# Optimization experiments

Hardware: AMD Instinct MI355X
Metric: run time of the kernel (lower is better)

Reference implementation:

```python
import jax, jax.numpy as jnp
import numpy as np

B, D, H, W, K = 32, 128, 128, 128, 32

def setup_inputs() -> dict:
    key = jax.random.key(0)
    k1, k2, k3 = jax.random.split(key, 3)
    X = jax.random.normal(k1, (B, D, H, W), dtype=jnp.float32)
    std1 = 1.0 / np.sqrt(K * D)
    codewords = jax.random.uniform(k2, (K, D), dtype=jnp.float32, minval=-std1, maxval=std1)
    scale = jax.random.uniform(k3, (K,), dtype=jnp.float32, minval=-1.0, maxval=0.0)
    return {"X": X, "codewords": codewords, "scale": scale}

def reference(X, codewords, scale):
    # X: [B, D, H, W] -> [B, N, D]
    b, d = X.shape[0], X.shape[1]
    x = X.reshape(b, d, -1).transpose(0, 2, 1)  # [B, N, D]
    x2 = jnp.sum(x * x, axis=-1, keepdims=True)            # [B, N, 1]
    c2 = jnp.sum(codewords * codewords, axis=-1)           # [K]
    xc = jnp.einsum('bnd,kd->bnk', x, codewords)           # [B, N, K]
    sl = scale * (x2 - 2.0 * xc + c2)                      # [B, N, K]
    A = jax.nn.softmax(sl, axis=2)                         # assignment weights
    # E[b,k,d] = sum_n A[b,n,k] * (x[b,n,d] - c[k,d])
    E = jnp.einsum('bnk,bnd->bkd', A, x) - jnp.sum(A, axis=1)[..., None] * codewords
    return E
```

## Files before the change

kernel.cpp:

```cpp
#include <hip/hip_runtime.h>
#include <hip/hip_bf16.h>

#define B_   32
#define D_   128
#define N_   16384
#define K_   32
#define NS   128
#define XS_STRIDE 136
#define AST_STRIDE 136

#define WS_WBF  0
#define WS_SC   2048
#define WS_C2S  2080
#define WS_EP   2112

typedef __attribute__((ext_vector_type(8))) short bf16x8;
typedef __attribute__((ext_vector_type(4))) float f32x4;

static __device__ inline unsigned int pk2(float lo, float hi) {
    __hip_bfloat162 h = __float22bfloat162_rn(make_float2(lo, hi));
    unsigned int r;
    __builtin_memcpy(&r, &h, 4);
    return r;
}

static __device__ inline bf16x8 pack8v(f32x4 a, f32x4 b) {
    union { unsigned int u[4]; bf16x8 f; } r;
    r.u[0] = pk2(a[0], a[1]);
    r.u[1] = pk2(a[2], a[3]);
    r.u[2] = pk2(b[0], b[1]);
    r.u[3] = pk2(b[2], b[3]);
    return r.f;
}

__global__ void prep_kernel(const float* __restrict__ cw,
                            const float* __restrict__ scale,
                            float* __restrict__ ws) {
    const int k = blockIdx.x;
    const int l = threadIdx.x;
    const float sc = scale[k] * 1.44269504088896f;
    unsigned short* Wbf = (unsigned short*)(ws + WS_WBF);
    float s = 0.f;
#pragma unroll
    for (int i = 0; i < 2; ++i) {
        const int d = l + i * 64;
        const float v = cw[k * D_ + d];
        s += v * v;
        const float w = -2.f * sc * v;
        unsigned int u = __float_as_uint(w);
        u += 0x7fffu + ((u >> 16) & 1u);
        Wbf[k * D_ + d] = (unsigned short)(u >> 16);
    }
#pragma unroll
    for (int o = 32; o > 0; o >>= 1) s += __shfl_down(s, o, 64);
    if (l == 0) {
        ws[WS_SC  + k] = sc;
        ws[WS_C2S + k] = sc * s;
    }
}

template<int NCHUNKT>
__global__ __launch_bounds__(256, 3) void main_kernel(
        const float* __restrict__ X,
        const float* __restrict__ ws_ro,
        float* __restrict__ AsumP,
        float* __restrict__ Ep)
{
    constexpr int CSZT  = N_ / NCHUNKT;
    constexpr int NSUBT = CSZT / NS;

    __shared__ __align__(16) unsigned short Xs[NS * XS_STRIDE];
    __shared__ __align__(16) unsigned short AsT[K_ * AST_STRIDE];

    const int t    = threadIdx.x;
    const int lane = t & 63;
    const int w    = t >> 6;
    const int mc   = lane & 15;
    const int q    = lane >> 4;

    const int blk   = blockIdx.x;
    const int b     = blk / NCHUNKT;
    const int chunk = blk % NCHUNKT;
    const int n0    = chunk * CSZT;

    const float* Xb = X + (size_t)b * ((size_t)D_ * N_);

    const unsigned short* Wbf = (const unsigned short*)(ws_ro + WS_WBF);
    bf16x8 wf[2][4];
#pragma unroll
    for (int kb = 0; kb < 2; ++kb)
#pragma unroll
        for (int kd = 0; kd < 4; ++kd)
            wf[kb][kd] = *(const bf16x8*)&Wbf[(kb * 16 + mc) * D_ + kd * 32 + q * 8];

    float scr[2][4], c2r[2][4];
#pragma unroll
    for (int kb = 0; kb < 2; ++kb)
#pragma unroll
        for (int r = 0; r < 4; ++r) {
            scr[kb][r] = ws_ro[WS_SC  + kb * 16 + q * 4 + r];
            c2r[kb][r] = ws_ro[WS_C2S + kb * 16 + q * 4 + r];
        }

    bf16x8 ones;
#pragma unroll
    for (int i = 0; i < 8; ++i) ones[i] = (short)0x3F80;

    f32x4 accE[2][2] = {{{0.f,0.f,0.f,0.f},{0.f,0.f,0.f,0.f}},
                        {{0.f,0.f,0.f,0.f},{0.f,0.f,0.f,0.f}}};
    f32x4 accO[2]    = {{0.f,0.f,0.f,0.f},{0.f,0.f,0.f,0.f}};

    const float* xr0 = Xb + (size_t)(w * 32 + mc) * N_ + n0 + q * 8;
    const int dA = w * 32 + mc;

    for (int s = 0; s < NSUBT; ++s) {
        const float* xp = xr0 + s * NS;
        bf16x8 xf0[4], xf1[4];
#pragma unroll
        for (int ks = 0; ks < 4; ++ks) {
            const f32x4 a0 = *(const f32x4*)(xp + ks * 32);
            const f32x4 b0 = *(const f32x4*)(xp + ks * 32 + 4);
            const f32x4 a1 = *(const f32x4*)(xp + ks * 32 + (size_t)16 * N_);
            const f32x4 b1 = *(const f32x4*)(xp + ks * 32 + (size_t)16 * N_ + 4);
            xf0[ks] = pack8v(a0, b0);
            xf1[ks] = pack8v(a1, b1);
        }
#pragma unroll
        for (int ks = 0; ks < 4; ++ks) {
            union { bf16x8 f; unsigned int u[4]; } ua, ub;
            ua.f = xf0[ks];
            ub.f = xf1[ks];
            const int base = (ks * 32 + q * 8) * XS_STRIDE + dA;
#pragma unroll
            for (int j2 = 0; j2 < 4; ++j2) {
                Xs[base + (2*j2)   * XS_STRIDE]      = (unsigned short)(ua.u[j2]);
                Xs[base + (2*j2+1) * XS_STRIDE]      = (unsigned short)(ua.u[j2] >> 16);
                Xs[base + (2*j2)   * XS_STRIDE + 16] = (unsigned short)(ub.u[j2]);
                Xs[base + (2*j2+1) * XS_STRIDE + 16] = (unsigned short)(ub.u[j2] >> 16);
            }
        }
        __syncthreads();

#pragma unroll
        for (int cb = 0; cb < NS / 64; ++cb) {
            const int ntl  = (w * (NS / 64) + cb) * 16;
            const int rowb = (ntl + mc) * XS_STRIDE;

            union fr { bf16x8 f; unsigned int u[4]; } xb[4];
#pragma unroll
            for (int kd = 0; kd < 4; ++kd)
                xb[kd].f = *(const bf16x8*)&Xs[rowb + kd * 32 + q * 8];

            float x2 = 0.f;
#pragma unroll
            for (int kd = 0; kd < 4; ++kd)
#pragma unroll
                for (int wd = 0; wd < 4; ++wd) {
                    const float lo = __uint_as_float(xb[kd].u[wd] << 16);
                    const float hi = __uint_as_float(xb[kd].u[wd] & 0xffff0000u);
                    x2 = fmaf(lo, lo, x2);
                    x2 = fmaf(hi, hi, x2);
                }

            f32x4 S0 = {0.f,0.f,0.f,0.f};
            f32x4 S1 = {0.f,0.f,0.f,0.f};
#pragma unroll
            for (int kd = 0; kd < 4; ++kd) {
                S0 = __builtin_amdgcn_mfma_f32_16x16x32_bf16(wf[0][kd], xb[kd].f, S0, 0, 0, 0);
                S1 = __builtin_amdgcn_mfma_f32_16x16x32_bf16(wf[1][kd], xb[kd].f, S1, 0, 0, 0);
            }

            x2 += __shfl_xor(x2, 16, 64);
            x2 += __shfl_xor(x2, 32, 64);

            float sl[8];
#pragma unroll
            for (int r = 0; r < 4; ++r) {
                sl[r]     = fmaf(scr[0][r], x2, S0[r] + c2r[0][r]);
                sl[4 + r] = fmaf(scr[1][r], x2, S1[r] + c2r[1][r]);
            }
            float m = sl[0];
#pragma unroll
            for (int i = 1; i < 8; ++i) m = fmaxf(m, sl[i]);
            m = fmaxf(m, __shfl_xor(m, 16, 64));
            m = fmaxf(m, __shfl_xor(m, 32, 64));
            float ssum = 0.f;
#pragma unroll
            for (int i = 0; i < 8; ++i) { sl[i] = exp2f(sl[i] - m); ssum += sl[i]; }
            ssum += __shfl_xor(ssum, 16, 64);
            ssum += __shfl_xor(ssum, 32, 64);
            const float inv = 1.f / ssum;

            const int col = ntl + mc;
#pragma unroll
            for (int r = 0; r < 4; ++r) {
                const unsigned int u = pk2(sl[r] * inv, sl[4 + r] * inv);
                AsT[(q * 4 + r) * AST_STRIDE + col]      = (unsigned short)u;
                AsT[(16 + q * 4 + r) * AST_STRIDE + col] = (unsigned short)(u >> 16);
            }
        }
        __syncthreads();

#pragma unroll
        for (int ks = 0; ks < NS / 32; ++ks) {
            const int nl = ks * 32 + q * 8;
            const bf16x8 a0 = *(const bf16x8*)&AsT[mc * AST_STRIDE + nl];
            const bf16x8 a1 = *(const bf16x8*)&AsT[(16 + mc) * AST_STRIDE + nl];
            accE[0][0] = __builtin_amdgcn_mfma_f32_16x16x32_bf16(a0, xf0[ks], accE[0][0], 0, 0, 0);
            accE[0][1] = __builtin_amdgcn_mfma_f32_16x16x32_bf16(a0, xf1[ks], accE[0][1], 0, 0, 0);
            accE[1][0] = __builtin_amdgcn_mfma_f32_16x16x32_bf16(a1, xf0[ks], accE[1][0], 0, 0, 0);
            accE[1][1] = __builtin_amdgcn_mfma_f32_16x16x32_bf16(a1, xf1[ks], accE[1][1], 0, 0, 0);
            if (w == 0) {
                accO[0] = __builtin_amdgcn_mfma_f32_16x16x32_bf16(a0, ones, accO[0], 0, 0, 0);
                accO[1] = __builtin_amdgcn_mfma_f32_16x16x32_bf16(a1, ones, accO[1], 0, 0, 0);
            }
        }
    }

    float* EpB = Ep + (size_t)blk * (K_ * D_);
#pragma unroll
    for (int kh = 0; kh < 2; ++kh)
#pragma unroll
        for (int ds = 0; ds < 2; ++ds)
#pragma unroll
            for (int r = 0; r < 4; ++r) {
                const int k = kh * 16 + q * 4 + r;
                const int d = w * 32 + ds * 16 + mc;
                EpB[k * D_ + d] = accE[kh][ds][r];
            }
    if (w == 0 && mc == 0) {
#pragma unroll
        for (int kh = 0; kh < 2; ++kh)
#pragma unroll
            for (int r = 0; r < 4; ++r)
                AsumP[blk * K_ + kh * 16 + q * 4 + r] = accO[kh][r];
    }
}

template<int NCHUNKT>
__global__ void finalize_kernel(const float* __restrict__ cw,
                                const float* __restrict__ AsumP,
                                const float* __restrict__ Ep,
                                float* __restrict__ out)
{
    const int idx = blockIdx.x * 256 + threadIdx.x;
    const int d = idx & 127;
    const int k = (idx >> 7) & 31;
    const int b = idx >> 12;
    float s = 0.f, asum = 0.f;
#pragma unroll
    for (int c = 0; c < NCHUNKT; ++c) {
        const int blk = b * NCHUNKT + c;
        s    += Ep[(size_t)blk * (K_ * D_) + k * D_ + d];
        asum += AsumP[blk * K_ + k];
    }
    out[idx] = s - asum * cw[k * D_ + d];
}

extern "C" void kernel_launch(void* const* d_in, const int* in_sizes, int n_in,
                              void* d_out, int out_size, void* d_ws, size_t ws_size,
                              hipStream_t stream) {
    const float* X     = (const float*)d_in[0];
    const float* cw    = (const float*)d_in[1];
    const float* scale = (const float*)d_in[2];
    float* out = (float*)d_out;
    float* ws  = (float*)d_ws;

    prep_kernel<<<K_, 64, 0, stream>>>(cw, scale, ws);

    const size_t need32 = (size_t)(WS_EP + 1024 * (K_ * D_) + 1024 * K_) * 4;
    if (ws_size >= need32) {
        float* Ep    = ws + WS_EP;
        float* AsumP = Ep + (size_t)1024 * (K_ * D_);
        main_kernel<32><<<B_ * 32, 256, 0, stream>>>(X, ws, AsumP, Ep);
        finalize_kernel<32><<<(B_ * K_ * D_) / 256, 256, 0, stream>>>(cw, AsumP, Ep, out);
    } else {
        float* Ep    = ws + WS_EP;
        float* AsumP = Ep + (size_t)512 * (K_ * D_);
        main_kernel<16><<<B_ * 16, 256, 0, stream>>>(X, ws, AsumP, Ep);
        finalize_kernel<16><<<(B_ * K_ * D_) / 256, 256, 0, stream>>>(cw, AsumP, Ep, out);
    }
}
```

Before: 396.7 us.

## Double-buffer X register loads with smaller sub-tile and swizzled LDS layout

Halves the inner sub-tile from 128 to 64 points and prefetches the next sub-tile's global loads into a second register buffer while the current one is packed and processed. The LDS column index for X is XOR-style rotated by the row quarter to reduce bank conflicts on both the transposed stores and the fragment reads. Occupancy hint drops from 3 to 2 blocks per CU to make room for the extra prefetch registers, and the loop is fully unrolled. The smaller tile doubles the number of barriers per chunk.

```diff
diff --git a/kernel.cpp b/kernel.cpp
--- a/kernel.cpp
+++ b/kernel.cpp
@@ -5,9 +5,9 @@
 #define D_   128
 #define N_   16384
 #define K_   32
-#define NS   128
+#define NS   64
 #define XS_STRIDE 136
-#define AST_STRIDE 136
+#define AST_STRIDE 72
 
 #define WS_WBF  0
 #define WS_SC   2048
@@ -60,7 +60,7 @@
 }
 
 template<int NCHUNKT>
-__global__ __launch_bounds__(256, 3) void main_kernel(
+__global__ __launch_bounds__(256, 2) void main_kernel(
         const float* __restrict__ X,
         const float* __restrict__ ws_ro,
         float* __restrict__ AsumP,
@@ -113,43 +113,58 @@
     const float* xr0 = Xb + (size_t)(w * 32 + mc) * N_ + n0 + q * 8;
     const int dA = w * 32 + mc;
 
+    auto do_loads = [&](f32x4 (&dst)[8], int sidx) {
+        const float* xp = xr0 + sidx * NS;
+#pragma unroll
+        for (int ks = 0; ks < 2; ++ks) {
+            dst[ks * 4 + 0] = *(const f32x4*)(xp + ks * 32);
+            dst[ks * 4 + 1] = *(const f32x4*)(xp + ks * 32 + 4);
+            dst[ks * 4 + 2] = *(const f32x4*)(xp + ks * 32 + (size_t)16 * N_);
+            dst[ks * 4 + 3] = *(const f32x4*)(xp + ks * 32 + (size_t)16 * N_ + 4);
+        }
+    };
+
+    f32x4 ld[2][8];
+    do_loads(ld[0], 0);
+
+#pragma unroll
     for (int s = 0; s < NSUBT; ++s) {
-        const float* xp = xr0 + s * NS;
-        bf16x8 xf0[4], xf1[4];
-#pragma unroll
-        for (int ks = 0; ks < 4; ++ks) {
-            const f32x4 a0 = *(const f32x4*)(xp + ks * 32);
-            const f32x4 b0 = *(const f32x4*)(xp + ks * 32 + 4);
-            const f32x4 a1 = *(const f32x4*)(xp + ks * 32 + (size_t)16 * N_);
-            const f32x4 b1 = *(const f32x4*)(xp + ks * 32 + (size_t)16 * N_ + 4);
-            xf0[ks] = pack8v(a0, b0);
-            xf1[ks] = pack8v(a1, b1);
-        }
-#pragma unroll
-        for (int ks = 0; ks < 4; ++ks) {
+        if (s + 1 < NSUBT) do_loads(ld[(s + 1) & 1], s + 1);
+
+        bf16x8 xf0[2], xf1[2];
+#pragma unroll
+        for (int ks = 0; ks < 2; ++ks) {
+            xf0[ks] = pack8v(ld[s & 1][ks * 4 + 0], ld[s & 1][ks * 4 + 1]);
+            xf1[ks] = pack8v(ld[s & 1][ks * 4 + 2], ld[s & 1][ks * 4 + 3]);
+        }
+#pragma unroll
+        for (int ks = 0; ks < 2; ++ks) {
             union { bf16x8 f; unsigned int u[4]; } ua, ub;
             ua.f = xf0[ks];
             ub.f = xf1[ks];
-            const int base = (ks * 32 + q * 8) * XS_STRIDE + dA;
+            const int rbase = (ks * 32 + q * 8) * XS_STRIDE;
+            const int ca  = (dA      + (q << 4)) & 127;
+            const int cb2 = (dA + 16 + (q << 4)) & 127;
 #pragma unroll
             for (int j2 = 0; j2 < 4; ++j2) {
-                Xs[base + (2*j2)   * XS_STRIDE]      = (unsigned short)(ua.u[j2]);
-                Xs[base + (2*j2+1) * XS_STRIDE]      = (unsigned short)(ua.u[j2] >> 16);
-                Xs[base + (2*j2)   * XS_STRIDE + 16] = (unsigned short)(ub.u[j2]);
-                Xs[base + (2*j2+1) * XS_STRIDE + 16] = (unsigned short)(ub.u[j2] >> 16);
+                Xs[rbase + (2*j2)   * XS_STRIDE + ca]  = (unsigned short)(ua.u[j2]);
+                Xs[rbase + (2*j2+1) * XS_STRIDE + ca]  = (unsigned short)(ua.u[j2] >> 16);
+                Xs[rbase + (2*j2)   * XS_STRIDE + cb2] = (unsigned short)(ub.u[j2]);
+                Xs[rbase + (2*j2+1) * XS_STRIDE + cb2] = (unsigned short)(ub.u[j2] >> 16);
             }
         }
         __syncthreads();
 
-#pragma unroll
-        for (int cb = 0; cb < NS / 64; ++cb) {
-            const int ntl  = (w * (NS / 64) + cb) * 16;
-            const int rowb = (ntl + mc) * XS_STRIDE;
+        {
+            const int ntl  = w * 16;
+            const int row  = ntl + mc;
+            const int rowb = row * XS_STRIDE;
+            const int qn   = (row >> 3) & 3;
 
             union fr { bf16x8 f; unsigned int u[4]; } xb[4];
 #pragma unroll
             for (int kd = 0; kd < 4; ++kd)
-                xb[kd].f = *(const bf16x8*)&Xs[rowb + kd * 32 + q * 8];
+                xb[kd].f = *(const bf16x8*)&Xs[rowb + ((kd * 32 + q * 8 + (qn << 4)) & 127)];
 
             float x2 = 0.f;
 #pragma unroll
@@ -202,7 +217,7 @@
         __syncthreads();
 
 #pragma unroll
-        for (int ks = 0; ks < NS / 32; ++ks) {
+        for (int ks = 0; ks < 2; ++ks) {
             const int nl = ks * 32 + q * 8;
             const bf16x8 a0 = *(const bf16x8*)&AsT[mc * AST_STRIDE + nl];
             const bf16x8 a1 = *(const bf16x8*)&AsT[(16 + mc) * AST_STRIDE + nl];
```

Result: faster. 370.3 us (-6.6%).
